# Kernel optimization log

Hardware: AMD Instinct MI355X
Metric: run time of the kernel (lower is better)

## Reference

```python
import jax, jax.numpy as jnp
import numpy as np

N_NODES = 50000
DEG = 32
N_EDGES = N_NODES * DEG
NODE_FT_DIM = 64  # hardcoded in original forward
ALPHA = 0.2


def setup_inputs() -> dict:
    key = jax.random.key(0)
    ks = jax.random.split(key, 8)
    node_fts = jax.random.normal(ks[0], (N_NODES, 256), dtype=jnp.float32)
    edge_fts = jax.random.normal(ks[1], (N_EDGES, 32), dtype=jnp.float32)
    # edges sorted by source, fixed degree -> matches original repeat_interleave semantics
    src = jnp.repeat(jnp.arange(N_NODES, dtype=jnp.int64), DEG)
    dst = jax.random.randint(ks[2], (N_EDGES,), 0, N_NODES, dtype=jnp.int64)
    edges = jnp.stack([src, dst], axis=1)
    W_node = jax.random.normal(ks[3], (256, 64), dtype=jnp.float32) * 0.06
    W_edge = jax.random.normal(ks[4], (32, 64), dtype=jnp.float32) * 0.14
    a_node = jax.random.normal(ks[5], (128, 1), dtype=jnp.float32) * 0.12
    a_edge = jax.random.normal(ks[6], (128, 1), dtype=jnp.float32) * 0.12
    return {"node_fts": node_fts, "edge_fts": edge_fts, "edges": edges,
            "W_node": W_node, "W_edge": W_edge, "a_node": a_node, "a_edge": a_edge}


def _leaky(x):
    return jnp.where(x >= 0, x, ALPHA * x)


def reference(node_fts, edge_fts, edges, W_node, W_edge, a_node, a_edge):
    n_nodes = node_fts.shape[0]
    src, dst = edges[:, 0], edges[:, 1]
    edge_fts_padded = jnp.pad(edge_fts, ((0, 0), (0, NODE_FT_DIM - edge_fts.shape[1])))

    h_v = node_fts @ W_node   # [N, 64]
    e_v = edge_fts @ W_edge   # [E, 64]

    # attention logits: [h_src || h_dst] @ a_node == h@a1 gathered + h@a2 gathered
    a_n1, a_n2 = a_node[:NODE_FT_DIM, 0], a_node[NODE_FT_DIM:, 0]
    a_e1, a_e2 = a_edge[:NODE_FT_DIM, 0], a_edge[NODE_FT_DIM:, 0]
    node_att = _leaky((h_v @ a_n1)[src] + (h_v @ a_n2)[dst])          # [E]
    # edge branch replaces slot 1 with padded edge features
    edge_att = _leaky((h_v @ a_e1)[src] + edge_fts_padded @ a_e2)      # [E]

    def seg_softmax(att):
        w = jnp.exp(jnp.clip(att, -2.0, 2.0))
        denom = jax.ops.segment_sum(w, src, num_segments=n_nodes)
        return w / denom[src]

    node_att_norm = seg_softmax(node_att)
    edge_att_norm = seg_softmax(edge_att)
    node_att_var = jnp.var(node_att_norm, ddof=1)
    edge_att_var = jnp.var(edge_att_norm, ddof=1)

    node_out = jax.ops.segment_sum(h_v[dst] * node_att_norm[:, None], src, num_segments=n_nodes)
    # original indexes e_v (per-edge rows) with node indices dst; in-range since E > N
    edge_out = jax.ops.segment_sum(e_v[dst] * edge_att_norm[:, None], src, num_segments=n_nodes)
    return node_out, edge_out, node_att_var, edge_att_var
```

## Files before the change

### kernel.cpp

```cpp
#include <hip/hip_runtime.h>
#include <hip/hip_fp16.h>

#define ALPHA 0.2f
static constexpr int NN = 50000;
static constexpr long NE = (long)NN * 32;

typedef float f4v __attribute__((ext_vector_type(4)));
typedef float f2v __attribute__((ext_vector_type(2)));

static constexpr long WS_HN1 = 0;
static constexpr long WS_HN2 = NN;
static constexpr long WS_HE1 = 2L * NN;
static constexpr long WS_ST  = 3L * NN;
static constexpr long WS_P   = 5L * NN;
static constexpr long WS_HEV = 5L * NN + 512;

__global__ __launch_bounds__(256) void k_hv(const float* __restrict__ A,
                                            const float* __restrict__ W,
                                            const float* __restrict__ a_node,
                                            const float* __restrict__ a_edge,
                                            __half* __restrict__ hev,
                                            float* __restrict__ hn1,
                                            float* __restrict__ hn2,
                                            float* __restrict__ he1) {
    __shared__ float As[16][65];
    __shared__ float Ws[16][64];
    const int t  = threadIdx.x;
    const int m0 = blockIdx.x * 64;
    const int tr = t >> 4, tc = t & 15;
    const int lr = t >> 2, seg = t & 3;
    const int wk = t >> 4, wc = t & 15;

    float acc[4][4] = {};
    for (int k0 = 0; k0 < 256; k0 += 16) {
        int row = m0 + lr;
        f4v av = {0.f, 0.f, 0.f, 0.f};
        if (row < NN)
            av = __builtin_nontemporal_load(
                     reinterpret_cast<const f4v*>(&A[(long)row * 256 + k0 + seg * 4]));
        As[seg*4+0][lr] = av.x; As[seg*4+1][lr] = av.y;
        As[seg*4+2][lr] = av.z; As[seg*4+3][lr] = av.w;
        *reinterpret_cast<float4*>(&Ws[wk][wc*4]) =
            *reinterpret_cast<const float4*>(&W[(k0 + wk) * 64 + wc * 4]);
        __syncthreads();
        #pragma unroll
        for (int kk = 0; kk < 16; ++kk) {
            float a0 = As[kk][tr*4+0], a1 = As[kk][tr*4+1];
            float a2 = As[kk][tr*4+2], a3 = As[kk][tr*4+3];
            float b0 = Ws[kk][tc*4+0], b1 = Ws[kk][tc*4+1];
            float b2 = Ws[kk][tc*4+2], b3 = Ws[kk][tc*4+3];
            acc[0][0] += a0*b0; acc[0][1] += a0*b1; acc[0][2] += a0*b2; acc[0][3] += a0*b3;
            acc[1][0] += a1*b0; acc[1][1] += a1*b1; acc[1][2] += a1*b2; acc[1][3] += a1*b3;
            acc[2][0] += a2*b0; acc[2][1] += a2*b1; acc[2][2] += a2*b2; acc[2][3] += a2*b3;
            acc[3][0] += a3*b0; acc[3][1] += a3*b1; acc[3][2] += a3*b2; acc[3][3] += a3*b3;
        }
        __syncthreads();
    }

    float an1[4], an2[4], ae1[4];
    #pragma unroll
    for (int j = 0; j < 4; ++j) {
        an1[j] = a_node[tc*4 + j];
        an2[j] = a_node[64 + tc*4 + j];
        ae1[j] = a_edge[tc*4 + j];
    }

    #pragma unroll
    for (int q = 0; q < 4; ++q) {
        float p1 = 0.f, p2 = 0.f, p3 = 0.f;
        #pragma unroll
        for (int j = 0; j < 4; ++j) {
            p1 += acc[q][j] * an1[j];
            p2 += acc[q][j] * an2[j];
            p3 += acc[q][j] * ae1[j];
        }
        #pragma unroll
        for (int m = 1; m <= 8; m <<= 1) {
            p1 += __shfl_xor(p1, m);
            p2 += __shfl_xor(p2, m);
            p3 += __shfl_xor(p3, m);
        }
        int row = m0 + tr * 4 + q;
        if (row < NN) {
            ushort4 hp;
            hp.x = __half_as_ushort(__float2half(acc[q][0]));
            hp.y = __half_as_ushort(__float2half(acc[q][1]));
            hp.z = __half_as_ushort(__float2half(acc[q][2]));
            hp.w = __half_as_ushort(__float2half(acc[q][3]));
            *reinterpret_cast<ushort4*>(&hev[(long)row * 128 + tc * 4]) = hp;
            if (tc == 0) { hn1[row] = p1; hn2[row] = p2; he1[row] = p3; }
        }
    }
}

__global__ __launch_bounds__(256) void k_ev(const float* __restrict__ ef,
                                            const float* __restrict__ We,
                                            __half* __restrict__ hev) {
    const int lane = threadIdx.x & 63, w = threadIdx.x >> 6;
    const int r = blockIdx.x * 4 + w;
    float acc = 0.f;
    #pragma unroll
    for (int k = 0; k < 32; ++k)
        acc += ef[(long)r * 32 + k] * We[k * 64 + lane];
    hev[(long)r * 128 + 64 + lane] = __float2half(acc);
}

__global__ __launch_bounds__(256) void k_edge(const float* __restrict__ ef,
                                              const int*   __restrict__ edges,
                                              const float* __restrict__ a_edge,
                                              const float* __restrict__ hn1,
                                              const float* __restrict__ hn2,
                                              const float* __restrict__ he1,
                                              const __half* __restrict__ hev,
                                              float* __restrict__ st,
                                              float* __restrict__ out) {
    const int t = threadIdx.x;
    const int w = t >> 6, l = t & 63;
    const int n = blockIdx.x * 4 + w;
    const int i = l >> 1, h = l & 1;
    const long ebase = (long)n * 32;

    const f4v* efb = reinterpret_cast<const f4v*>(&ef[(ebase + i) * 32 + h * 16]);
    float dot = 0.f;
    #pragma unroll
    for (int j = 0; j < 4; ++j) {
        f4v v = __builtin_nontemporal_load(efb + j);
        float4 a = *reinterpret_cast<const float4*>(&a_edge[64 + h * 16 + j * 4]);
        dot += v.x*a.x + v.y*a.y + v.z*a.z + v.w*a.w;
    }
    dot += __shfl_xor(dot, 1);

    const int d = __builtin_nontemporal_load(&edges[(ebase + i) * 2 + 1]);

    float attn = hn1[n] + hn2[d];
    attn = attn >= 0.f ? attn : ALPHA * attn;
    float wn = __expf(fminf(fmaxf(attn, -2.f), 2.f));

    float atte = he1[n] + dot;
    atte = atte >= 0.f ? atte : ALPHA * atte;
    float we = __expf(fminf(fmaxf(atte, -2.f), 2.f));

    float dn = wn, de = we;
    #pragma unroll
    for (int m = 2; m <= 32; m <<= 1) { dn += __shfl_xor(dn, m); de += __shfl_xor(de, m); }
    float nn = wn / dn, ne = we / de;

    float sqn = nn * nn, sqe = ne * ne;
    #pragma unroll
    for (int m = 2; m <= 32; m <<= 1) { sqn += __shfl_xor(sqn, m); sqe += __shfl_xor(sqe, m); }
    if (l == 0) { st[n] = sqn; st[NN + n] = sqe; }

    const bool isE = l >= 32;
    float a0 = 0.f, a1 = 0.f;
    #pragma unroll
    for (int b = 0; b < 4; ++b) {
        int dv[8]; float wn8[8], we8[8]; __half2 h2[8];
        #pragma unroll
        for (int u = 0; u < 8; ++u) {
            const int e2 = (b * 8 + u) * 2;
            dv[u]  = __builtin_amdgcn_readlane(d, e2);
            wn8[u] = __int_as_float(__builtin_amdgcn_readlane(__float_as_int(nn), e2));
            we8[u] = __int_as_float(__builtin_amdgcn_readlane(__float_as_int(ne), e2));
            h2[u]  = *reinterpret_cast<const __half2*>(&hev[(long)dv[u] * 128 + l * 2]);
        }
        #pragma unroll
        for (int u = 0; u < 8; ++u) {
            float wt = isE ? we8[u] : wn8[u];
            float2 f = __half22float2(h2[u]);
            a0 = fmaf(wt, f.x, a0);
            a1 = fmaf(wt, f.y, a1);
        }
    }
    long off = isE ? ((long)NN * 64 + (long)n * 64 + (l - 32) * 2)
                   : ((long)n * 64 + l * 2);
    f2v r; r.x = a0; r.y = a1;
    __builtin_nontemporal_store(r, reinterpret_cast<f2v*>(&out[off]));
}

__global__ __launch_bounds__(256) void k_red1(const float* __restrict__ st,
                                              float* __restrict__ part) {
    const int t = threadIdx.x;
    const int n = blockIdx.x * 256 + t;
    float v0 = 0.f, v1 = 0.f;
    if (n < NN) { v0 = st[n]; v1 = st[NN + n]; }
    #pragma unroll
    for (int m = 1; m <= 32; m <<= 1) { v0 += __shfl_xor(v0, m); v1 += __shfl_xor(v1, m); }
    __shared__ float ls[4][2];
    const int wv = t >> 6;
    if ((t & 63) == 0) { ls[wv][0] = v0; ls[wv][1] = v1; }
    __syncthreads();
    if (t == 0) {
        part[(long)blockIdx.x * 2]     = ls[0][0] + ls[1][0] + ls[2][0] + ls[3][0];
        part[(long)blockIdx.x * 2 + 1] = ls[0][1] + ls[1][1] + ls[2][1] + ls[3][1];
    }
}

__global__ __launch_bounds__(64) void k_red2(const float* __restrict__ part,
                                             float* __restrict__ out) {
    const int t = threadIdx.x;
    double v0 = 0.0, v1 = 0.0;
    for (int b = t; b < 196; b += 64) {
        v0 += (double)part[b * 2];
        v1 += (double)part[b * 2 + 1];
    }
    #pragma unroll
    for (int m = 1; m <= 32; m <<= 1) { v0 += __shfl_xor(v0, m); v1 += __shfl_xor(v1, m); }
    if (t == 0) {
        const double M = (double)NE;
        const double corr = (double)NN * (double)NN / M;
        out[6400000] = (float)((v0 - corr) / (M - 1.0));
        out[6400001] = (float)((v1 - corr) / (M - 1.0));
    }
}

extern "C" void kernel_launch(void* const* d_in, const int* in_sizes, int n_in,
                              void* d_out, int out_size, void* d_ws, size_t ws_size,
                              hipStream_t stream) {
    const float* node_fts = (const float*)d_in[0];
    const float* edge_fts = (const float*)d_in[1];
    const int*   edges    = (const int*)  d_in[2];
    const float* W_node   = (const float*)d_in[3];
    const float* W_edge   = (const float*)d_in[4];
    const float* a_node   = (const float*)d_in[5];
    const float* a_edge   = (const float*)d_in[6];
    float* out = (float*)d_out;
    float* ws  = (float*)d_ws;

    float*  hn1 = ws + WS_HN1;
    float*  hn2 = ws + WS_HN2;
    float*  he1 = ws + WS_HE1;
    float*  st  = ws + WS_ST;
    float*  prt = ws + WS_P;
    __half* hev = (__half*)(ws + WS_HEV);

    k_hv  <<<(NN + 63) / 64, 256, 0, stream>>>(node_fts, W_node, a_node, a_edge,
                                               hev, hn1, hn2, he1);
    k_ev  <<<NN / 4, 256, 0, stream>>>(edge_fts, W_edge, hev);
    k_edge<<<NN / 4, 256, 0, stream>>>(edge_fts, edges, a_edge, hn1, hn2, he1,
                                       hev, st, out);
    k_red1<<<196, 256, 0, stream>>>(st, prt);
    k_red2<<<1, 64, 0, stream>>>(prt, out);
}
```

Before: 174.3 us.

## Split edge kernel into attention and gather passes with packed per-edge records

The fused edge kernel is split in two. k_att computes the softmax weights and writes a packed record per edge: the dst index plus both weights as half2. k_gather then reads those records and does the weighted row gathers from hev. The aim is to separate the latency-bound streaming phase from the random-gather phase so each can reach higher occupancy. The split costs an extra 12.8MB write and read of records, an extra launch, and rounding of the weights to fp16. It also reorders k_ev before k_hv and drops the nontemporal load on node_fts.

```diff
diff --git a/kernel.cpp b/kernel.cpp
--- a/kernel.cpp
+++ b/kernel.cpp
@@ -7,13 +7,15 @@
 
 typedef float f4v __attribute__((ext_vector_type(4)));
 typedef float f2v __attribute__((ext_vector_type(2)));
+typedef unsigned int u2v __attribute__((ext_vector_type(2)));
 
 static constexpr long WS_HN1 = 0;
 static constexpr long WS_HN2 = NN;
 static constexpr long WS_HE1 = 2L * NN;
 static constexpr long WS_ST  = 3L * NN;
 static constexpr long WS_P   = 5L * NN;
-static constexpr long WS_HEV = 5L * NN + 512;
+static constexpr long WS_REC = 5L * NN + 512;
+static constexpr long WS_HEV = WS_REC + 2L * NE;
 
 __global__ __launch_bounds__(256) void k_hv(const float* __restrict__ A,
                                             const float* __restrict__ W,
@@ -34,10 +36,9 @@
     float acc[4][4] = {};
     for (int k0 = 0; k0 < 256; k0 += 16) {
         int row = m0 + lr;
-        f4v av = {0.f, 0.f, 0.f, 0.f};
+        float4 av = make_float4(0.f, 0.f, 0.f, 0.f);
         if (row < NN)
-            av = __builtin_nontemporal_load(
-                     reinterpret_cast<const f4v*>(&A[(long)row * 256 + k0 + seg * 4]));
+            av = *reinterpret_cast<const float4*>(&A[(long)row * 256 + k0 + seg * 4]);
         As[seg*4+0][lr] = av.x; As[seg*4+1][lr] = av.y;
         As[seg*4+2][lr] = av.z; As[seg*4+3][lr] = av.w;
         *reinterpret_cast<float4*>(&Ws[wk][wc*4]) =
@@ -105,15 +106,14 @@
     hev[(long)r * 128 + 64 + lane] = __float2half(acc);
 }
 
-__global__ __launch_bounds__(256) void k_edge(const float* __restrict__ ef,
-                                              const int*   __restrict__ edges,
-                                              const float* __restrict__ a_edge,
-                                              const float* __restrict__ hn1,
-                                              const float* __restrict__ hn2,
-                                              const float* __restrict__ he1,
-                                              const __half* __restrict__ hev,
-                                              float* __restrict__ st,
-                                              float* __restrict__ out) {
+__global__ __launch_bounds__(256) void k_att(const float* __restrict__ ef,
+                                             const int*   __restrict__ edges,
+                                             const float* __restrict__ a_edge,
+                                             const float* __restrict__ hn1,
+                                             const float* __restrict__ hn2,
+                                             const float* __restrict__ he1,
+                                             u2v* __restrict__ rec,
+                                             float* __restrict__ st) {
     const int t = threadIdx.x;
     const int w = t >> 6, l = t & 63;
     const int n = blockIdx.x * 4 + w;
@@ -150,22 +150,40 @@
     for (int m = 2; m <= 32; m <<= 1) { sqn += __shfl_xor(sqn, m); sqe += __shfl_xor(sqe, m); }
     if (l == 0) { st[n] = sqn; st[NN + n] = sqe; }
 
+    if (h == 0) {
+        __half2 p = __floats2half2_rn(nn, ne);
+        u2v r;
+        r.x = (unsigned int)d;
+        r.y = *reinterpret_cast<unsigned int*>(&p);
+        __builtin_nontemporal_store(r, &rec[ebase + i]);
+    }
+}
+
+__global__ __launch_bounds__(256) void k_gather(const u2v* __restrict__ rec,
+                                                const __half* __restrict__ hev,
+                                                float* __restrict__ out) {
+    const int t = threadIdx.x;
+    const int w = t >> 6, l = t & 63;
+    const int n = blockIdx.x * 4 + w;
+
+    u2v r = __builtin_nontemporal_load(&rec[(long)n * 32 + (l & 31)]);
+
     const bool isE = l >= 32;
     float a0 = 0.f, a1 = 0.f;
     #pragma unroll
     for (int b = 0; b < 4; ++b) {
-        int dv[8]; float wn8[8], we8[8]; __half2 h2[8];
+        int dv[8]; unsigned int wv[8]; __half2 h2[8];
         #pragma unroll
         for (int u = 0; u < 8; ++u) {
-            const int e2 = (b * 8 + u) * 2;
-            dv[u]  = __builtin_amdgcn_readlane(d, e2);
-            wn8[u] = __int_as_float(__builtin_amdgcn_readlane(__float_as_int(nn), e2));
-            we8[u] = __int_as_float(__builtin_amdgcn_readlane(__float_as_int(ne), e2));
-            h2[u]  = *reinterpret_cast<const __half2*>(&hev[(long)dv[u] * 128 + l * 2]);
+            const int ii = b * 8 + u;
+            dv[u] = __builtin_amdgcn_readlane((int)r.x, ii);
+            wv[u] = (unsigned int)__builtin_amdgcn_readlane((int)r.y, ii);
+            h2[u] = *reinterpret_cast<const __half2*>(&hev[(long)dv[u] * 128 + l * 2]);
         }
         #pragma unroll
         for (int u = 0; u < 8; ++u) {
-            float wt = isE ? we8[u] : wn8[u];
+            __half2 wp = *reinterpret_cast<__half2*>(&wv[u]);
+            float wt = isE ? __high2float(wp) : __low2float(wp);
             float2 f = __half22float2(h2[u]);
             a0 = fmaf(wt, f.x, a0);
             a1 = fmaf(wt, f.y, a1);
@@ -173,8 +191,8 @@
     }
     long off = isE ? ((long)NN * 64 + (long)n * 64 + (l - 32) * 2)
                    : ((long)n * 64 + l * 2);
-    f2v r; r.x = a0; r.y = a1;
-    __builtin_nontemporal_store(r, reinterpret_cast<f2v*>(&out[off]));
+    f2v o; o.x = a0; o.y = a1;
+    __builtin_nontemporal_store(o, reinterpret_cast<f2v*>(&out[off]));
 }
 
 __global__ __launch_bounds__(256) void k_red1(const float* __restrict__ st,
@@ -231,13 +249,15 @@
     float*  he1 = ws + WS_HE1;
     float*  st  = ws + WS_ST;
     float*  prt = ws + WS_P;
+    u2v*    rec = (u2v*)(ws + WS_REC);
     __half* hev = (__half*)(ws + WS_HEV);
 
-    k_hv  <<<(NN + 63) / 64, 256, 0, stream>>>(node_fts, W_node, a_node, a_edge,
-                                               hev, hn1, hn2, he1);
-    k_ev  <<<NN / 4, 256, 0, stream>>>(edge_fts, W_edge, hev);
-    k_edge<<<NN / 4, 256, 0, stream>>>(edge_fts, edges, a_edge, hn1, hn2, he1,
-                                       hev, st, out);
-    k_red1<<<196, 256, 0, stream>>>(st, prt);
-    k_red2<<<1, 64, 0, stream>>>(prt, out);
-}
+    k_ev    <<<NN / 4, 256, 0, stream>>>(edge_fts, W_edge, hev);
+    k_hv    <<<(NN + 63) / 64, 256, 0, stream>>>(node_fts, W_node, a_node, a_edge,
+                                                 hev, hn1, hn2, he1);
+    k_att   <<<NN / 4, 256, 0, stream>>>(edge_fts, edges, a_edge, hn1, hn2, he1,
+                                         rec, st);
+    k_gather<<<NN / 4, 256, 0, stream>>>(rec, hev, out);
+    k_red1  <<<196, 256, 0, stream>>>(st, prt);
+    k_red2  <<<1, 64, 0, stream>>>(prt, out);
+}
```

Measured after the change: 200.3 us. +14.9%, slower.
